# Kernel optimization log

Measured on AMD Instinct MI355X. Metric: run time of the kernel, lower is better.

## Reference

```python
import jax, jax.numpy as jnp
import numpy as np

SMOOTH = 1.0
MAX_DIST = 10


def _neighbor_conv(x):
    # 3x3 ones kernel with zero center, padding=1 (NCHW, C=1)
    k = jnp.ones((1, 1, 3, 3), x.dtype).at[0, 0, 1, 1].set(0.0)
    return jax.lax.conv_general_dilated(
        x, k, window_strides=(1, 1), padding=[(1, 1), (1, 1)],
        dimension_numbers=('NCHW', 'OIHW', 'NCHW'))


def _analyze_skeleton(skel):
    n = _neighbor_conv(skel)
    on = skel > 0.5
    endpoints = ((n == 1) & on).astype(skel.dtype)
    midpoints = ((n == 2) & on).astype(skel.dtype)
    junctions = ((n > 2) & on).astype(skel.dtype)
    return endpoints, midpoints, junctions


def _iou(p, g):
    inter = jnp.sum(p * g, axis=(2, 3))
    union = jnp.sum(p, axis=(2, 3)) + jnp.sum(g, axis=(2, 3)) - inter
    return (inter + SMOOTH) / (union + SMOOTH)


def _structural_similarity(pred_skel, gt_skel):
    pe, pm, pj = _analyze_skeleton(pred_skel)
    ge, gm, gj = _analyze_skeleton(gt_skel)
    e_iou, m_iou, j_iou = _iou(pe, ge), _iou(pm, gm), _iou(pj, gj)
    ge_c = jnp.sum(ge, axis=(2, 3))
    gj_c = jnp.sum(gj, axis=(2, 3))
    gm_c = jnp.sum(gm, axis=(2, 3))
    total = ge_c + gj_c + gm_c + SMOOTH
    loss = 1.0 - ((ge_c / total) * e_iou + (gj_c / total) * j_iou + (gm_c / total) * m_iou)
    return loss.mean()


def _maxpool3(x):
    return jax.lax.reduce_window(
        x, -jnp.inf, jax.lax.max,
        window_dimensions=(1, 1, 3, 3), window_strides=(1, 1, 1, 1),
        padding=[(0, 0), (0, 0), (1, 1), (1, 1)])


def _distance_approximation(target, reference):
    # Fixed MAX_DIST iterations; identical math to the torch early-exit loop
    # because new_points requires ~found_mask (no distance is overwritten).
    tgt_on = target > 0.5

    def step(carry, d):
        dilated, found, dist = carry
        dilated = _maxpool3(dilated)
        new = (dilated > 0.5) & tgt_on & (~found)
        dist = dist + d.astype(dist.dtype) * new.astype(dist.dtype)
        return (dilated, found | new, dist), None

    init = (reference, jnp.zeros(target.shape, bool), jnp.zeros_like(target))
    (_, found, dist), _ = jax.lax.scan(step, init, jnp.arange(1, MAX_DIST + 1, dtype=jnp.int32))
    unfound = tgt_on & (~found)
    dist = dist + jnp.asarray(MAX_DIST, dist.dtype) * unfound.astype(dist.dtype)
    total_points = jnp.sum(tgt_on.astype(dist.dtype), axis=(2, 3))
    return jnp.sum(dist, axis=(2, 3)) / (total_points + SMOOTH)


def _medial_axis_distance(pred_skel, gt_skel):
    p2g = _distance_approximation(pred_skel, gt_skel)
    g2p = _distance_approximation(gt_skel, pred_skel)
    return (((p2g + g2p) / 2.0) / MAX_DIST).mean()


def setup_inputs() -> dict:
    key = jax.random.key(0)
    k1, k2 = jax.random.split(key)
    B, C, H, W = 32, 1, 512, 512
    pred_skel = jax.random.uniform(k1, (B, C, H, W), dtype=jnp.float32)
    gt_skel = (jax.random.uniform(k2, (B, C, H, W), dtype=jnp.float32) < 0.1).astype(jnp.float32)
    return {"pred_skel": pred_skel, "gt_skel": gt_skel}


def reference(pred_skel, gt_skel):
    inter = jnp.sum(pred_skel * gt_skel, axis=(2, 3))
    psum = jnp.sum(pred_skel, axis=(2, 3))
    gsum = jnp.sum(gt_skel, axis=(2, 3))
    dice = (2.0 * inter + SMOOTH) / (psum + gsum + SMOOTH)
    dice_loss = 1.0 - dice.mean()
    structural_loss = _structural_similarity(pred_skel, gt_skel)
    medial_loss = _medial_axis_distance(pred_skel, gt_skel)
    avg_mag = (dice_loss + structural_loss + medial_loss) / 3.0
    bal_dice = dice_loss / (dice_loss + SMOOTH) * avg_mag
    bal_struct = structural_loss / (structural_loss + SMOOTH) * avg_mag
    bal_medial = medial_loss / (medial_loss + SMOOTH) * avg_mag
    return bal_dice + bal_struct + bal_medial
```

## Files before the change

### kernel.cpp

```cpp
#include <hip/hip_runtime.h>
#include <stdint.h>

#define BATCH 32
#define H 512
#define W 512
#define NACC 16
#define TH 32
#define HALO 9
#define RH (TH + 2*HALO)
#define NWORDS (RH*8)
#define NT 1024
#define NW (NT/64)
#define NTILE (H/TH)
#define NBLK (NTILE*BATCH)


__global__ __launch_bounds__(NT, 4) void fused_kernel(
    const float* __restrict__ pred, const float* __restrict__ gt,
    float* __restrict__ part)
{
    __shared__ uint64_t MpS[NWORDS + 2];
    __shared__ uint64_t MgS[NWORDS + 2];
    __shared__ uint64_t Ge[TH * 8];
    __shared__ uint64_t Gm[TH * 8];
    __shared__ uint64_t Gj[TH * 8];
    __shared__ float    EC[2][TH];
    __shared__ float    redf[NW][2];
    __shared__ unsigned redu[NW][6];

    uint64_t* Mp = MpS + 1;
    uint64_t* Mg = MgS + 1;

    int fid  = blockIdx.x;
    int b    = fid & 31;
    int tile = fid >> 5;

    const float* pimg = pred + (size_t)b * H * W;
    const float* gimg = gt   + (size_t)b * H * W;
    int y0 = tile * TH;
    int tid = threadIdx.x, lane = tid & 63, wid = tid >> 6;

    float v0 = 0.f, v1 = 0.f;
    for (int s0 = wid; s0 < NWORDS; s0 += 4 * NW) {
        float vp[4], vg[4];
        #pragma unroll
        for (int u = 0; u < 4; ++u) {
            int s = s0 + u * NW;
            vp[u] = 0.f; vg[u] = 0.f;
            int ry = y0 - HALO + (s >> 3);
            if (s < NWORDS && (unsigned)ry < (unsigned)H) {
                int i0 = ry * W + (s & 7) * 64 + lane;
                vp[u] = pimg[i0]; vg[u] = gimg[i0];
            }
        }
        #pragma unroll
        for (int u = 0; u < 4; ++u) {
            int s = s0 + u * NW;
            if (s < NWORDS) {
                unsigned long long mp = __ballot(vp[u] > 0.5f);
                unsigned long long mg = __ballot(vg[u] > 0.5f);
                if (lane == 0) { Mp[s] = mp; Mg[s] = mg; }
                int r = s >> 3;
                if (r >= HALO && r < HALO + TH) {
                    v1 += vp[u];
                    v0 += (vg[u] > 0.5f) ? vp[u] : 0.f;
                }
            }
        }
    }
    if (tid == 0) { MpS[0] = 0; MpS[NWORDS + 1] = 0; MgS[0] = 0; MgS[NWORDS + 1] = 0; }

    int qi = tid & 127, band = tid >> 7;
    int x4 = qi * 4;
    int ys = y0 + band * 4;
    float4 pm4 = make_float4(0, 0, 0, 0), pc4;
    if (ys > 0) pm4 = *(const float4*)(pimg + (size_t)(ys - 1) * W + x4);
    pc4 = *(const float4*)(pimg + (size_t)ys * W + x4);

    if (tid < 2 * TH) {
        int c = tid >> 5, r = tid & (TH - 1);
        int y = y0 + r, col = 255 + c;
        float sum = (y > 0     ? pimg[(size_t)(y - 1) * W + col] : 0.f)
                  +              pimg[(size_t)y * W + col]
                  + (y < H - 1 ? pimg[(size_t)(y + 1) * W + col] : 0.f);
        EC[c][r] = sum;
    }
    __syncthreads();

    unsigned cge = 0, cgm = 0, cgj = 0;
    if (tid < 256) {
        int r = tid >> 3, w = tid & 7;
        int oM = (HALO + r) * 8 + w;
        bool wl = (w > 0), wr = (w < 7);
        uint64_t A  = Mg[oM - 8], Bm = Mg[oM], Cm = Mg[oM + 8];
        uint64_t AL = wl ? Mg[oM - 9] : 0ULL, AR = wr ? Mg[oM - 7] : 0ULL;
        uint64_t BL = wl ? Mg[oM - 1] : 0ULL, BR = wr ? Mg[oM + 1] : 0ULL;
        uint64_t CL = wl ? Mg[oM + 7] : 0ULL, CR = wr ? Mg[oM + 9] : 0ULL;
        uint64_t Aw = (A  << 1) | (AL >> 63), Ae = (A  >> 1) | (AR << 63);
        uint64_t Bw = (Bm << 1) | (BL >> 63), Be = (Bm >> 1) | (BR << 63);
        uint64_t Cw = (Cm << 1) | (CL >> 63), Ce = (Cm >> 1) | (CR << 63);
        uint64_t c1, c2, c3, c5, t;
        t = Aw ^ A;  uint64_t s1 = t ^ Ae;  c1 = (Aw & A)  | (Ae & t);
        t = Bw ^ Be; uint64_t s2 = t ^ Cw;  c2 = (Bw & Be) | (Cw & t);
        t = Cm ^ Ce; uint64_t s3 = t ^ s1;  c3 = (Cm & Ce) | (s1 & t);
        uint64_t b0 = s2 ^ s3, c4 = s2 & s3;
        t = c1 ^ c2; uint64_t s5 = t ^ c3;  c5 = (c1 & c2) | (c3 & t);
        uint64_t b1 = s5 ^ c4, c6 = s5 & c4;
        uint64_t b2 = c5 ^ c6, b3 = c5 & c6;
        uint64_t nz23 = ~(b2 | b3);
        uint64_t ge = Bm & b0 & ~b1 & nz23;
        uint64_t gm = Bm & b1 & ~b0 & nz23;
        uint64_t gj = Bm & (b2 | b3 | (b1 & b0));
        Ge[tid] = ge; Gm[tid] = gm; Gj[tid] = gj;
        cge = (unsigned)__popcll(ge);
        cgm = (unsigned)__popcll(gm);
        cgj = (unsigned)__popcll(gj);
    }

    int dsum = 0, dcnt = 0;
    {
        const uint32_t* Mp32 = (const uint32_t*)Mp;
        const uint32_t* Mg32 = (const uint32_t*)Mg;
        bool isP = tid < 512;
        int di = tid & 511;
        int o  = (HALO + (di >> 4)) * 16 + (di & 15);
        int h  = di & 15;
        bool wL = (h > 0), wR = (h < 15);
        const uint32_t* MT = isP ? Mp32 : Mg32;
        const uint32_t* MV = isP ? Mg32 : Mp32;

        uint32_t T = MT[o];
        dcnt = __popc(T);
        dsum = dcnt;
        uint32_t VM = MV[o];
        uint32_t VL = wL ? MV[o - 1] : 0u;
        uint32_t VR = wR ? MV[o + 1] : 0u;
        uint32_t C = VM;

        #pragma unroll
        for (int a = 1; a <= 9; ++a) {
            int lo = o - 16 * a, hi = o + 16 * a;
            uint32_t NM = MV[lo] | MV[hi];
            uint32_t NL = wL ? (MV[lo - 1] | MV[hi - 1]) : 0u;
            uint32_t NR = wR ? (MV[lo + 1] | MV[hi + 1]) : 0u;
            uint32_t SL = NL, SM = NM, SR = NR;
            const int m = a - 1;
            if (m >= 1) {
                SM |= (SM << 1) | (SM >> 1) | (SL >> 31) | (SR << 31);
                SL |= SL << 1; SR |= SR >> 1;
            }
            if (m >= 2) {
                const int s = (m == 2) ? 1 : 2;
                SM |= (SM << s) | (SM >> s) | (SL >> (32 - s)) | (SR << (32 - s));
                SL |= SL << s; SR |= SR >> s;
            }
            if (m >= 4) {
                const int s = (m - 3 < 4) ? (m - 3) : 4;
                SM |= (SM << s) | (SM >> s) | (SL >> (32 - s)) | (SR << (32 - s));
                SL |= SL << s; SR |= SR >> s;
            }
            if (m >= 8) {
                const int s = m - 7;
                SM |= (SM << s) | (SM >> s) | (SL >> (32 - s)) | (SR << (32 - s));
                SL |= SL << s; SR |= SR >> s;
            }
            C |= SM;
            VL |= NL; VM |= NM; VR |= NR;
            C |= (VM << a) | (VM >> a) | (VL >> (32 - a)) | (VR << (32 - a));
            uint32_t rem = T & ~C;
            dsum += __popc(rem);
            if (__all(rem == 0u)) break;
        }
    }
    __syncthreads();

    uint64_t cpack = 0ULL;
    {
        int wdx = qi >> 4;
        int ss = (qi & 15) * 4;
        for (int r = 0; r < 4; ++r) {
            int y = ys + r;
            float4 pp4 = (y < H - 1) ? *(const float4*)(pimg + (size_t)(y + 1) * W + x4)
                                     : make_float4(0, 0, 0, 0);
            int ry = band * 4 + r;
            uint64_t gew = Ge[ry * 8 + wdx];
            uint64_t gmw = Gm[ry * 8 + wdx];
            uint64_t gjw = Gj[ry * 8 + wdx];

            float ps[6];
            ps[1] = pm4.x + pc4.x + pp4.x; ps[2] = pm4.y + pc4.y + pp4.y;
            ps[3] = pm4.z + pc4.z + pp4.z; ps[4] = pm4.w + pc4.w + pp4.w;
            float psl = __shfl_up(ps[4], 1, 64);
            float psr = __shfl_down(ps[1], 1, 64);
            if (lane == 0)  psl = (qi == 0)   ? 0.f : EC[0][ry];
            if (lane == 63) psr = (qi == 127) ? 0.f : EC[1][ry];
            ps[0] = psl; ps[5] = psr;

            float pcv[4] = {pc4.x, pc4.y, pc4.z, pc4.w};
            #pragma unroll
            for (int j = 0; j < 4; ++j) {
                float np = ps[j] + ps[j + 1] + ps[j + 2] - pcv[j];
                bool pon = pcv[j] > 0.5f;
                bool pe  = pon && (np == 1.f);
                bool pmb = pon && (np == 2.f);
                bool pjb = pon && (np > 2.f);
                unsigned geb = (unsigned)(gew >> (ss + j)) & 1u;
                unsigned gmb = (unsigned)(gmw >> (ss + j)) & 1u;
                unsigned gjb = (unsigned)(gjw >> (ss + j)) & 1u;
                cpack += (uint64_t)pe
                       | ((uint64_t)pmb << 7)
                       | ((uint64_t)pjb << 14)
                       | ((uint64_t)(pe  && geb) << 21)
                       | ((uint64_t)(pmb && gmb) << 28)
                       | ((uint64_t)(pjb && gjb) << 35);
            }
            pm4 = pc4; pc4 = pp4;
        }
    }

    unsigned c_pe = (unsigned)( cpack        & 0x7F);
    unsigned c_pm = (unsigned)((cpack >> 7 ) & 0x7F);
    unsigned c_pj = (unsigned)((cpack >> 14) & 0x7F);
    unsigned c_ie = (unsigned)((cpack >> 21) & 0x7F);
    unsigned c_im = (unsigned)((cpack >> 28) & 0x7F);
    unsigned c_ij = (unsigned)((cpack >> 35) & 0x7F);
    unsigned r0 = (unsigned)dsum | ((unsigned)dcnt << 16);
    unsigned r1 = c_pe | (c_pm << 16);
    unsigned r2 = c_pj | (c_ie << 16);
    unsigned r3 = c_im | (c_ij << 16);
    unsigned r4 = cge | (cgm << 16);
    unsigned r5 = cgj;
    #pragma unroll
    for (int off = 32; off; off >>= 1) {
        v0 += __shfl_down(v0, off, 64);
        v1 += __shfl_down(v1, off, 64);
        r0 += __shfl_down(r0, off, 64);
        r1 += __shfl_down(r1, off, 64);
        r2 += __shfl_down(r2, off, 64);
        r3 += __shfl_down(r3, off, 64);
        r4 += __shfl_down(r4, off, 64);
        r5 += __shfl_down(r5, off, 64);
    }
    if (lane == 0) {
        redf[wid][0] = v0; redf[wid][1] = v1;
        redu[wid][0] = r0; redu[wid][1] = r1; redu[wid][2] = r2;
        redu[wid][3] = r3; redu[wid][4] = r4; redu[wid][5] = r5;
    }
    __syncthreads();
    if (tid < 16) {
        int k = tid;
        float s = 0.f;
        if (k < 2) {
            #pragma unroll
            for (int wv = 0; wv < NW; ++wv) s += redf[wv][k];
        } else {
            static const uint8_t WB[16] = {0,0, 8, 0,0,0,  0,0,0, 0,0,0,   0,0,8,8};
            static const uint8_t WC[16] = {0,0, 8, 16,16,16, 4,4,4, 16,16,16, 8,8,8,8};
            static const uint8_t RG[16] = {0,0, 0, 1,1,2,  4,4,5, 2,3,3,   0,0,0,0};
            static const uint8_t HI[16] = {0,0, 1, 0,1,0,  0,1,0, 1,0,1,   0,1,0,1};
            unsigned u = 0;
            for (int wv = WB[k]; wv < WB[k] + WC[k]; ++wv)
                u += (redu[wv][RG[k]] >> (HI[k] * 16)) & 0xFFFFu;
            s = (float)u;
        }
        part[fid * NACC + k] = s;
    }
}

__global__ __launch_bounds__(512) void final_kernel(
    const float* __restrict__ part, float* __restrict__ out)
{
    __shared__ float sacc[BATCH][NACC];
    __shared__ float tri[BATCH][3];
    int t = threadIdx.x;
    {
        int b = t >> 4, k = t & 15;
        float s = 0.f;
        #pragma unroll 4
        for (int j = 0; j < NTILE; ++j)
            s += part[((j << 5) + b) * NACC + k];
        sacc[b][k] = s;
    }
    __syncthreads();
    if (t < BATCH) {
        const float* a = sacc[t];
        float inter = a[0], psum = a[1], gsum = a[2];
        float dice = (2.f * inter + 1.f) / (psum + gsum + 1.f);

        float pe = a[3], pm = a[4], pj = a[5];
        float ge = a[6], gm = a[7], gj = a[8];
        float ie = a[9], im = a[10], ij = a[11];
        float e_iou = (ie + 1.f) / (pe + ge - ie + 1.f);
        float m_iou = (im + 1.f) / (pm + gm - im + 1.f);
        float j_iou = (ij + 1.f) / (pj + gj - ij + 1.f);
        float total = ge + gj + gm + 1.f;
        float sloss = 1.f - ((ge / total) * e_iou + (gj / total) * j_iou + (gm / total) * m_iou);

        float p2g = a[12] / (a[13] + 1.f);
        float g2p = a[14] / (a[15] + 1.f);
        float med = ((p2g + g2p) * 0.5f) / 10.f;
        tri[t][0] = dice; tri[t][1] = sloss; tri[t][2] = med;
    }
    __syncthreads();
    if (t == 0) {
        float dice = 0.f, sloss = 0.f, med = 0.f;
        for (int b = 0; b < BATCH; ++b) {
            dice += tri[b][0]; sloss += tri[b][1]; med += tri[b][2];
        }
        float dice_loss  = 1.f - dice / (float)BATCH;
        float structural = sloss / (float)BATCH;
        float medial     = med / (float)BATCH;
        float avg = (dice_loss + structural + medial) / 3.f;
        float r = dice_loss  / (dice_loss  + 1.f) * avg
                + structural / (structural + 1.f) * avg
                + medial     / (medial     + 1.f) * avg;
        out[0] = r;
    }
}

extern "C" void kernel_launch(void* const* d_in, const int* in_sizes, int n_in,
                              void* d_out, int out_size, void* d_ws, size_t ws_size,
                              hipStream_t stream)
{
    const float* pred = (const float*)d_in[0];
    const float* gt   = (const float*)d_in[1];
    float* part = (float*)d_ws;
    float* out  = (float*)d_out;

    fused_kernel<<<dim3(NBLK), NT, 0, stream>>>(pred, gt, part);
    final_kernel<<<1, 512, 0, stream>>>(part, out);
}
```

Before: 111.6 us.

## Double row tile height per block to halve halo reloads and block count

Each block now handles 64 rows instead of 32, so the 9-row halo is loaded once for twice the useful rows and the grid has half as many blocks. The distance pass runs two halves per thread, and reduction bookkeeping is split so each half writes the same per-32-row partial slots as before, which leaves the final kernel unchanged. This cuts redundant global loads and ballot work on halos. The cost is less parallelism (256 blocks), longer per-thread serial work and more shared memory per block.

```diff
diff --git a/kernel.cpp b/kernel.cpp
--- a/kernel.cpp
+++ b/kernel.cpp
@@ -5,50 +5,49 @@
 #define H 512
 #define W 512
 #define NACC 16
-#define TH 32
+#define TH2 64
 #define HALO 9
-#define RH (TH + 2*HALO)
-#define NWORDS (RH*8)
+#define RH2 (TH2 + 2*HALO)
+#define NW2 (RH2*8)
 #define NT 1024
-#define NW (NT/64)
-#define NTILE (H/TH)
-#define NBLK (NTILE*BATCH)
+#define NW 16
+#define NTILE 16
+#define NBLK2 (BATCH * (H/TH2))
 
 
 __global__ __launch_bounds__(NT, 4) void fused_kernel(
     const float* __restrict__ pred, const float* __restrict__ gt,
     float* __restrict__ part)
 {
-    __shared__ uint64_t MpS[NWORDS + 2];
-    __shared__ uint64_t MgS[NWORDS + 2];
-    __shared__ uint64_t Ge[TH * 8];
-    __shared__ uint64_t Gm[TH * 8];
-    __shared__ uint64_t Gj[TH * 8];
-    __shared__ float    EC[2][TH];
-    __shared__ float    redf[NW][2];
-    __shared__ unsigned redu[NW][6];
+    __shared__ uint64_t MpS[NW2 + 2];
+    __shared__ uint64_t MgS[NW2 + 2];
+    __shared__ uint64_t Ge[TH2 * 8];
+    __shared__ uint64_t Gm[TH2 * 8];
+    __shared__ uint64_t Gj[TH2 * 8];
+    __shared__ float    EC[2][TH2];
+    __shared__ float    redfA[NW][2], redfB[NW][2];
+    __shared__ unsigned redu[NW][7];
 
     uint64_t* Mp = MpS + 1;
     uint64_t* Mg = MgS + 1;
 
     int fid  = blockIdx.x;
     int b    = fid & 31;
-    int tile = fid >> 5;
-
+    int t64  = fid >> 5;
     const float* pimg = pred + (size_t)b * H * W;
     const float* gimg = gt   + (size_t)b * H * W;
-    int y0 = tile * TH;
+    int y0 = t64 * TH2;
     int tid = threadIdx.x, lane = tid & 63, wid = tid >> 6;
 
-    float v0 = 0.f, v1 = 0.f;
-    for (int s0 = wid; s0 < NWORDS; s0 += 4 * NW) {
+    float v0A = 0.f, v1A = 0.f, v0B = 0.f, v1B = 0.f;
+    for (int s0 = wid; s0 < NW2; s0 += 4 * NW) {
         float vp[4], vg[4];
         #pragma unroll
         for (int u = 0; u < 4; ++u) {
             int s = s0 + u * NW;
             vp[u] = 0.f; vg[u] = 0.f;
             int ry = y0 - HALO + (s >> 3);
-            if (s < NWORDS && (unsigned)ry < (unsigned)H) {
+            if (s < NW2 && (unsigned)ry < (unsigned)H) {
                 int i0 = ry * W + (s & 7) * 64 + lane;
                 vp[u] = pimg[i0]; vg[u] = gimg[i0];
             }
@@ -56,29 +55,31 @@
         #pragma unroll
         for (int u = 0; u < 4; ++u) {
             int s = s0 + u * NW;
-            if (s < NWORDS) {
+            if (s < NW2) {
                 unsigned long long mp = __ballot(vp[u] > 0.5f);
                 unsigned long long mg = __ballot(vg[u] > 0.5f);
                 if (lane == 0) { Mp[s] = mp; Mg[s] = mg; }
-                int r = s >> 3;
-                if (r >= HALO && r < HALO + TH) {
-                    v1 += vp[u];
-                    v0 += (vg[u] > 0.5f) ? vp[u] : 0.f;
+                if (s >= 72 && s < 328) {
+                    v1A += vp[u];
+                    v0A += (vg[u] > 0.5f) ? vp[u] : 0.f;
+                } else if (s >= 328 && s < 584) {
+                    v1B += vp[u];
+                    v0B += (vg[u] > 0.5f) ? vp[u] : 0.f;
                 }
             }
         }
     }
-    if (tid == 0) { MpS[0] = 0; MpS[NWORDS + 1] = 0; MgS[0] = 0; MgS[NWORDS + 1] = 0; }
+    if (tid == 0) { MpS[0] = 0; MpS[NW2 + 1] = 0; MgS[0] = 0; MgS[NW2 + 1] = 0; }
 
     int qi = tid & 127, band = tid >> 7;
     int x4 = qi * 4;
-    int ys = y0 + band * 4;
+    int ys = y0 + band * 8;
     float4 pm4 = make_float4(0, 0, 0, 0), pc4;
     if (ys > 0) pm4 = *(const float4*)(pimg + (size_t)(ys - 1) * W + x4);
     pc4 = *(const float4*)(pimg + (size_t)ys * W + x4);
 
-    if (tid < 2 * TH) {
-        int c = tid >> 5, r = tid & (TH - 1);
+    if (tid < 2 * TH2) {
+        int c = tid >> 6, r = tid & (TH2 - 1);
         int y = y0 + r, col = 255 + c;
         float sum = (y > 0     ? pimg[(size_t)(y - 1) * W + col] : 0.f)
                   +              pimg[(size_t)y * W + col]
@@ -88,9 +89,9 @@
     __syncthreads();
 
     unsigned cge = 0, cgm = 0, cgj = 0;
-    if (tid < 256) {
-        int r = tid >> 3, w = tid & 7;
-        int oM = (HALO + r) * 8 + w;
+    if (tid < 512) {
+        int rr = tid >> 3, w = tid & 7;
+        int oM = (HALO + rr) * 8 + w;
         bool wl = (w > 0), wr = (w < 7);
         uint64_t A  = Mg[oM - 8], Bm = Mg[oM], Cm = Mg[oM + 8];
         uint64_t AL = wl ? Mg[oM - 9] : 0ULL, AR = wr ? Mg[oM - 7] : 0ULL;
@@ -117,59 +118,64 @@
         cgj = (unsigned)__popcll(gj);
     }
 
-    int dsum = 0, dcnt = 0;
+    int dsA = 0, dcA = 0, dsB = 0, dcB = 0;
     {
         const uint32_t* Mp32 = (const uint32_t*)Mp;
         const uint32_t* Mg32 = (const uint32_t*)Mg;
         bool isP = tid < 512;
         int di = tid & 511;
-        int o  = (HALO + (di >> 4)) * 16 + (di & 15);
         int h  = di & 15;
         bool wL = (h > 0), wR = (h < 15);
         const uint32_t* MT = isP ? Mp32 : Mg32;
         const uint32_t* MV = isP ? Mg32 : Mp32;
-
-        uint32_t T = MT[o];
-        dcnt = __popc(T);
-        dsum = dcnt;
-        uint32_t VM = MV[o];
-        uint32_t VL = wL ? MV[o - 1] : 0u;
-        uint32_t VR = wR ? MV[o + 1] : 0u;
-        uint32_t C = VM;
+        int oA = (HALO + (di >> 4)) * 16 + h;
 
         #pragma unroll
-        for (int a = 1; a <= 9; ++a) {
-            int lo = o - 16 * a, hi = o + 16 * a;
-            uint32_t NM = MV[lo] | MV[hi];
-            uint32_t NL = wL ? (MV[lo - 1] | MV[hi - 1]) : 0u;
-            uint32_t NR = wR ? (MV[lo + 1] | MV[hi + 1]) : 0u;
-            uint32_t SL = NL, SM = NM, SR = NR;
-            const int m = a - 1;
-            if (m >= 1) {
-                SM |= (SM << 1) | (SM >> 1) | (SL >> 31) | (SR << 31);
-                SL |= SL << 1; SR |= SR >> 1;
+        for (int half = 0; half < 2; ++half) {
+            int o = oA + half * (32 * 16);
+            uint32_t T = MT[o];
+            int dcnt = __popc(T);
+            int dsum = dcnt;
+            uint32_t VM = MV[o];
+            uint32_t VL = wL ? MV[o - 1] : 0u;
+            uint32_t VR = wR ? MV[o + 1] : 0u;
+            uint32_t C = VM;
+            #pragma unroll
+            for (int a = 1; a <= 9; ++a) {
+                int lo = o - 16 * a, hi = o + 16 * a;
+                uint32_t NM = MV[lo] | MV[hi];
+                uint32_t NL = wL ? (MV[lo - 1] | MV[hi - 1]) : 0u;
+                uint32_t NR = wR ? (MV[lo + 1] | MV[hi + 1]) : 0u;
+                uint32_t SL = NL, SM = NM, SR = NR;
+                const int m = a - 1;
+                if (m >= 1) {
+                    SM |= (SM << 1) | (SM >> 1) | (SL >> 31) | (SR << 31);
+                    SL |= SL << 1; SR |= SR >> 1;
+                }
+                if (m >= 2) {
+                    const int s = (m == 2) ? 1 : 2;
+                    SM |= (SM << s) | (SM >> s) | (SL >> (32 - s)) | (SR << (32 - s));
+                    SL |= SL << s; SR |= SR >> s;
+                }
+                if (m >= 4) {
+                    const int s = (m - 3 < 4) ? (m - 3) : 4;
+                    SM |= (SM << s) | (SM >> s) | (SL >> (32 - s)) | (SR << (32 - s));
+                    SL |= SL << s; SR |= SR >> s;
+                }
+                if (m >= 8) {
+                    const int s = m - 7;
+                    SM |= (SM << s) | (SM >> s) | (SL >> (32 - s)) | (SR << (32 - s));
+                    SL |= SL << s; SR |= SR >> s;
+                }
+                C |= SM;
+                VL |= NL; VM |= NM; VR |= NR;
+                C |= (VM << a) | (VM >> a) | (VL >> (32 - a)) | (VR << (32 - a));
+                uint32_t rem = T & ~C;
+                dsum += __popc(rem);
+                if (__all(rem == 0u)) break;
             }
-            if (m >= 2) {
-                const int s = (m == 2) ? 1 : 2;
-                SM |= (SM << s) | (SM >> s) | (SL >> (32 - s)) | (SR << (32 - s));
-                SL |= SL << s; SR |= SR >> s;
-            }
-            if (m >= 4) {
-                const int s = (m - 3 < 4) ? (m - 3) : 4;
-                SM |= (SM << s) | (SM >> s) | (SL >> (32 - s)) | (SR << (32 - s));
-                SL |= SL << s; SR |= SR >> s;
-            }
-            if (m >= 8) {
-                const int s = m - 7;
-                SM |= (SM << s) | (SM >> s) | (SL >> (32 - s)) | (SR << (32 - s));
-                SL |= SL << s; SR |= SR >> s;
-            }
-            C |= SM;
-            VL |= NL; VM |= NM; VR |= NR;
-            C |= (VM << a) | (VM >> a) | (VL >> (32 - a)) | (VR << (32 - a));
-            uint32_t rem = T & ~C;
-            dsum += __popc(rem);
-            if (__all(rem == 0u)) break;
+            if (half == 0) { dsA = dsum; dcA = dcnt; }
+            else           { dsB = dsum; dcB = dcnt; }
         }
     }
     __syncthreads();
@@ -178,22 +184,22 @@
     {
         int wdx = qi >> 4;
         int ss = (qi & 15) * 4;
-        for (int r = 0; r < 4; ++r) {
+        for (int r = 0; r < 8; ++r) {
             int y = ys + r;
             float4 pp4 = (y < H - 1) ? *(const float4*)(pimg + (size_t)(y + 1) * W + x4)
                                      : make_float4(0, 0, 0, 0);
-            int ry = band * 4 + r;
-            uint64_t gew = Ge[ry * 8 + wdx];
-            uint64_t gmw = Gm[ry * 8 + wdx];
-            uint64_t gjw = Gj[ry * 8 + wdx];
+            int rr = band * 8 + r;
+            uint64_t gew = Ge[rr * 8 + wdx];
+            uint64_t gmw = Gm[rr * 8 + wdx];
+            uint64_t gjw = Gj[rr * 8 + wdx];
 
             float ps[6];
             ps[1] = pm4.x + pc4.x + pp4.x; ps[2] = pm4.y + pc4.y + pp4.y;
             ps[3] = pm4.z + pc4.z + pp4.z; ps[4] = pm4.w + pc4.w + pp4.w;
             float psl = __shfl_up(ps[4], 1, 64);
             float psr = __shfl_down(ps[1], 1, 64);
-            if (lane == 0)  psl = (qi == 0)   ? 0.f : EC[0][ry];
-            if (lane == 63) psr = (qi == 127) ? 0.f : EC[1][ry];
+            if (lane == 0)  psl = (qi == 0)   ? 0.f : EC[0][rr];
+            if (lane == 63) psr = (qi == 127) ? 0.f : EC[1][rr];
             ps[0] = psl; ps[5] = psr;
 
             float pcv[4] = {pc4.x, pc4.y, pc4.z, pc4.w};
@@ -224,46 +230,64 @@
     unsigned c_ie = (unsigned)((cpack >> 21) & 0x7F);
     unsigned c_im = (unsigned)((cpack >> 28) & 0x7F);
     unsigned c_ij = (unsigned)((cpack >> 35) & 0x7F);
-    unsigned r0 = (unsigned)dsum | ((unsigned)dcnt << 16);
+    unsigned r0 = (unsigned)dsA | ((unsigned)dcA << 16);
     unsigned r1 = c_pe | (c_pm << 16);
     unsigned r2 = c_pj | (c_ie << 16);
     unsigned r3 = c_im | (c_ij << 16);
     unsigned r4 = cge | (cgm << 16);
     unsigned r5 = cgj;
+    unsigned r6 = (unsigned)dsB | ((unsigned)dcB << 16);
     #pragma unroll
     for (int off = 32; off; off >>= 1) {
-        v0 += __shfl_down(v0, off, 64);
-        v1 += __shfl_down(v1, off, 64);
+        v0A += __shfl_down(v0A, off, 64);
+        v1A += __shfl_down(v1A, off, 64);
+        v0B += __shfl_down(v0B, off, 64);
+        v1B += __shfl_down(v1B, off, 64);
         r0 += __shfl_down(r0, off, 64);
         r1 += __shfl_down(r1, off, 64);
         r2 += __shfl_down(r2, off, 64);
         r3 += __shfl_down(r3, off, 64);
         r4 += __shfl_down(r4, off, 64);
         r5 += __shfl_down(r5, off, 64);
+        r6 += __shfl_down(r6, off, 64);
     }
     if (lane == 0) {
-        redf[wid][0] = v0; redf[wid][1] = v1;
+        redfA[wid][0] = v0A; redfA[wid][1] = v1A;
+        redfB[wid][0] = v0B; redfB[wid][1] = v1B;
         redu[wid][0] = r0; redu[wid][1] = r1; redu[wid][2] = r2;
         redu[wid][3] = r3; redu[wid][4] = r4; redu[wid][5] = r5;
-    }
-    __syncthreads();
-    if (tid < 16) {
-        int k = tid;
+        redu[wid][6] = r6;
+    }
+    __syncthreads();
+    if (tid < 32) {
+        int sub = tid >> 4, k = tid & 15;
+        int fidT = (((t64 << 1) | sub) << 5) | b;
         float s = 0.f;
         if (k < 2) {
+            const float (*rf)[2] = sub ? redfB : redfA;
             #pragma unroll
-            for (int wv = 0; wv < NW; ++wv) s += redf[wv][k];
+            for (int wv = 0; wv < NW; ++wv) s += rf[wv][k];
         } else {
-            static const uint8_t WB[16] = {0,0, 8, 0,0,0,  0,0,0, 0,0,0,   0,0,8,8};
-            static const uint8_t WC[16] = {0,0, 8, 16,16,16, 4,4,4, 16,16,16, 8,8,8,8};
-            static const uint8_t RG[16] = {0,0, 0, 1,1,2,  4,4,5, 2,3,3,   0,0,0,0};
-            static const uint8_t HI[16] = {0,0, 1, 0,1,0,  0,1,0, 1,0,1,   0,1,0,1};
+            static const uint8_t WB[2][16] = {
+                {0,0, 8, 0,0,0, 0,0,0, 0,0,0, 0,0,8,8},
+                {0,0, 8, 8,8,8, 4,4,4, 8,8,8, 0,0,8,8}};
+            static const uint8_t WC[2][16] = {
+                {0,0, 8, 8,8,8, 4,4,4, 8,8,8, 8,8,8,8},
+                {0,0, 8, 8,8,8, 4,4,4, 8,8,8, 8,8,8,8}};
+            static const uint8_t RG[2][16] = {
+                {0,0, 0, 1,1,2, 4,4,5, 2,3,3, 0,0,0,0},
+                {0,0, 6, 1,1,2, 4,4,5, 2,3,3, 6,6,6,6}};
+            static const uint8_t HI[2][16] = {
+                {0,0, 1, 0,1,0, 0,1,0, 1,0,1, 0,1,0,1},
+                {0,0, 1, 0,1,0, 0,1,0, 1,0,1, 0,1,0,1}};
             unsigned u = 0;
-            for (int wv = WB[k]; wv < WB[k] + WC[k]; ++wv)
-                u += (redu[wv][RG[k]] >> (HI[k] * 16)) & 0xFFFFu;
+            int wb = WB[sub][k], wc = WC[sub][k];
+            int rg = RG[sub][k], hi = HI[sub][k];
+            for (int wv = wb; wv < wb + wc; ++wv)
+                u += (redu[wv][rg] >> (hi * 16)) & 0xFFFFu;
             s = (float)u;
         }
-        part[fid * NACC + k] = s;
+        part[fidT * NACC + k] = s;
     }
 }
 
@@ -327,6 +351,6 @@
     float* part = (float*)d_ws;
     float* out  = (float*)d_out;
 
-    fused_kernel<<<dim3(NBLK), NT, 0, stream>>>(pred, gt, part);
+    fused_kernel<<<dim3(NBLK2), NT, 0, stream>>>(pred, gt, part);
     final_kernel<<<1, 512, 0, stream>>>(part, out);
 }
```

New measurement: 110.5 us (median of 2 runs). Within noise of the previous version (-1.0%).
